# Kernel tuning notes

Hardware: AMD Instinct MI355X
Metric: run time of the kernel (lower is better)

Reference implementation:

```python
import jax, jax.numpy as jnp
import numpy as np

N = 50000
E = 800000
DIM = 64
MAX_DEG = 64
NUM_LAB = 16
BN_EPS = 1e-5
SLOPE = 0.01


def lrelu(x):
    return jnp.where(x > 0, x, SLOPE * x)


def batchnorm(x, w, b):
    m = x.mean(axis=0)
    v = x.var(axis=0)  # biased, matches torch BN normalization
    return (x - m) * jax.lax.rsqrt(v + BN_EPS) * w + b


def gin_conv(x, src, dst, wa, ba, wb, bb):
    # GINConv (eps=0): mlp(x + sum_{j->i} x_j); mlp = lin -> lrelu -> lin
    agg = jax.ops.segment_sum(x[src], dst, num_segments=x.shape[0])
    h = x + agg
    h = lrelu(h @ wa.T + ba)
    return h @ wb.T + bb


def setup_inputs() -> dict:
    key = jax.random.key(0)
    ks = iter(jax.random.split(key, 64))
    f = lambda *s: (jax.random.normal(next(ks), s, dtype=jnp.float32) * 0.1)
    dims = [2 * DIM, DIM, DIM, DIM]  # [128,64,64,64]
    inp = {
        'emb_deg': f(MAX_DEG, DIM),
        'emb_lab': f(NUM_LAB, DIM),
    }
    for i, (n1, n2) in enumerate(zip(dims[:-1], dims[1:])):
        inp[f'w{i}a'] = f(n1, n1)
        inp[f'b{i}a'] = f(n1)
        inp[f'w{i}b'] = f(n2, n1)
        inp[f'b{i}b'] = f(n2)
        inp[f'bn{i}_w'] = f(n2) + 1.0
        inp[f'bn{i}_b'] = f(n2)
    S = sum(dims)  # 320
    inp['fc1_w'] = f(DIM, S)
    inp['fc1_b'] = f(DIM)
    inp['fcbn_w'] = f(DIM) + 1.0
    inp['fcbn_b'] = f(DIM)
    inp['fc2_w'] = f(1, DIM)
    inp['fc2_b'] = f(1)
    inp['node_deg'] = jax.random.randint(next(ks), (N,), 0, MAX_DEG)
    inp['node_lab'] = jax.random.randint(next(ks), (N,), 0, NUM_LAB)
    inp['edge_index'] = jax.random.randint(next(ks), (2, E), 0, N)
    return inp


def reference(emb_deg, emb_lab,
              w0a, b0a, w0b, b0b, bn0_w, bn0_b,
              w1a, b1a, w1b, b1b, bn1_w, bn1_b,
              w2a, b2a, w2b, b2b, bn2_w, bn2_b,
              fc1_w, fc1_b, fcbn_w, fcbn_b, fc2_w, fc2_b,
              node_deg, node_lab, edge_index):
    src, dst = edge_index[0], edge_index[1]
    x0 = jnp.concatenate([emb_deg[node_deg], emb_lab[node_lab]], axis=1)  # [N, 2*DIM]
    z = [x0]
    layers = [(w0a, b0a, w0b, b0b, bn0_w, bn0_b),
              (w1a, b1a, w1b, b1b, bn1_w, bn1_b),
              (w2a, b2a, w2b, b2b, bn2_w, bn2_b)]
    for wa, ba, wb, bb, gw, gb in layers:
        x = gin_conv(z[-1], src, dst, wa, ba, wb, bb)
        x = lrelu(batchnorm(x, gw, gb))
        z.append(x)
    x = jnp.concatenate(z, axis=1)  # [N, sum(dims)]
    h = x @ fc1_w.T + fc1_b
    h = lrelu(batchnorm(h, fcbn_w, fcbn_b))
    out = jax.nn.sigmoid(h @ fc2_w.T + fc2_b)
    return out.squeeze(-1)  # [N]
```

## Files before the change

kernel.cpp:

```cpp
#include <hip/hip_runtime.h>

#define N_NODES 50000
#define E_EDGES 800000
#define BN_EPS 1e-5f
#define SLOPE 0.01f

#define SCAN_CHUNK 2048
#define SCAN_BLOCKS ((N_NODES + SCAN_CHUNK - 1) / SCAN_CHUNK)
#define STAT_SHARDS 32

typedef unsigned short ushort_t;
typedef unsigned int uint_t;
typedef short short8 __attribute__((ext_vector_type(8)));
typedef float floatx4 __attribute__((ext_vector_type(4)));

__device__ __forceinline__ float ulo(uint_t v) { return __uint_as_float(v << 16); }
__device__ __forceinline__ float uhi(uint_t v) { return __uint_as_float(v & 0xffff0000u); }
__device__ __forceinline__ ushort_t f2b(float f) {
    uint_t u = __float_as_uint(f);
    return (ushort_t)((u + 0x7fffu + ((u >> 16) & 1u)) >> 16);
}
__device__ __forceinline__ uint_t pack2(float a, float b) {
    return (uint_t)f2b(a) | ((uint_t)f2b(b) << 16);
}

#define OWA0 0
#define OWB0 16384
#define OWA1 24576
#define OWB1 28672
#define OWA2 32768
#define OWB2 36864
#define OFC1 40960
#define WTOT 61440
#define CVT_BLOCKS ((WTOT + 255) / 256)
#define P_BLOCKS 48

__global__ void k_prep(const float* __restrict__ wa0, const float* __restrict__ wb0,
                       const float* __restrict__ wa1, const float* __restrict__ wb1,
                       const float* __restrict__ wa2, const float* __restrict__ wb2,
                       const float* __restrict__ fc1w, ushort_t* __restrict__ dst,
                       const float* __restrict__ ed, const float* __restrict__ el,
                       ushort_t* __restrict__ Pt) {
    int b = blockIdx.x, t = threadIdx.x;
    if (b < CVT_BLOCKS) {
        int i = b * 256 + t;
        if (i >= WTOT) return;
        float v;
        if      (i < OWB0) v = wa0[i];
        else if (i < OWA1) v = wb0[i - OWB0];
        else if (i < OWB1) v = wa1[i - OWA1];
        else if (i < OWA2) v = wb1[i - OWB1];
        else if (i < OWB2) v = wa2[i - OWA2];
        else if (i < OFC1) v = wb2[i - OWB2];
        else               v = fc1w[i - OFC1];
        dst[i] = f2b(v);
    } else {
        int pid = (b - CVT_BLOCKS) * 256 + t;
        int c = pid >> 7, j = pid & 127;
        float acc = 0.f;
        if (c < 64) {
            const float* dr = ed + c * 64;
            const float* wr = wa0 + (size_t)j * 128;
            #pragma unroll 8
            for (int k = 0; k < 64; ++k) acc += dr[k] * wr[k];
        } else if (c < 80) {
            const float* dr = el + (c - 64) * 64;
            const float* wr = wa0 + (size_t)j * 128 + 64;
            #pragma unroll 8
            for (int k = 0; k < 64; ++k) acc += dr[k] * wr[k];
        }
        Pt[(size_t)j * 96 + c] = f2b(acc);
    }
}

__global__ void k_build_x0(const float* __restrict__ ed, const float* __restrict__ el,
                           const int* __restrict__ nd, const int* __restrict__ nl,
                           uint_t* __restrict__ x0u, int* __restrict__ ncls) {
    int idx = blockIdx.x * blockDim.x + threadIdx.x;
    if (idx >= N_NODES * 64) return;
    int n = idx >> 6, c = idx & 63;
    int d = nd[n], l = nl[n];
    if (c == 0) ncls[n] = d | (l << 16);
    float2 v = (c < 32) ? *(const float2*)(ed + d * 64 + c * 2)
                        : *(const float2*)(el + l * 64 + (c - 32) * 2);
    x0u[(size_t)n * 64 + c] = pack2(v.x, v.y);
}

__global__ void k_deg(const int* __restrict__ dst, int* __restrict__ deg) {
    int e = blockIdx.x * blockDim.x + threadIdx.x;
    if (e >= E_EDGES) return;
    atomicAdd(&deg[dst[e]], 1);
}

__global__ __launch_bounds__(256) void k_scan_a(const int* __restrict__ deg,
                                                int* __restrict__ bsum) {
    __shared__ int wsum[4];
    int t = threadIdx.x, b = blockIdx.x;
    int base = b * SCAN_CHUNK + t * 8;
    int s = 0;
    #pragma unroll
    for (int i = 0; i < 8; ++i) {
        int idx = base + i;
        if (idx < N_NODES) s += deg[idx];
    }
    #pragma unroll
    for (int o = 32; o; o >>= 1) s += __shfl_down(s, o);
    if ((t & 63) == 0) wsum[t >> 6] = s;
    __syncthreads();
    if (t == 0) bsum[b] = wsum[0] + wsum[1] + wsum[2] + wsum[3];
}

__global__ void k_scan_b(const int* __restrict__ bsum, int* __restrict__ bofs) {
    int t = threadIdx.x;
    int v = (t < SCAN_BLOCKS) ? bsum[t] : 0;
    int inc = v;
    #pragma unroll
    for (int o = 1; o < 32; o <<= 1) {
        int u = __shfl_up(inc, o, 32);
        if ((t & 31) >= o) inc += u;
    }
    if (t < SCAN_BLOCKS) bofs[t] = inc - v;
}

__global__ __launch_bounds__(256) void k_scan_c(const int* __restrict__ deg,
        const int* __restrict__ bofs, int* __restrict__ rowptr, int* __restrict__ wptr) {
    __shared__ int part[256];
    int t = threadIdx.x, b = blockIdx.x;
    int base = b * SCAN_CHUNK + t * 8;
    int vals[8];
    int s = 0;
    #pragma unroll
    for (int i = 0; i < 8; ++i) {
        int idx = base + i;
        vals[i] = (idx < N_NODES) ? deg[idx] : 0;
        s += vals[i];
    }
    part[t] = s;
    __syncthreads();
    #pragma unroll
    for (int off = 1; off < 256; off <<= 1) {
        int v = (t >= off) ? part[t - off] : 0;
        __syncthreads();
        part[t] += v;
        __syncthreads();
    }
    int run = bofs[b] + part[t] - s;
    #pragma unroll
    for (int i = 0; i < 8; ++i) {
        int idx = base + i;
        if (idx < N_NODES) {
            rowptr[idx] = run;
            wptr[idx]   = run;
            run += vals[i];
        }
    }
}

__global__ void k_fill(const int* __restrict__ src, const int* __restrict__ dst,
                       const int* __restrict__ ncls,
                       int* __restrict__ wptr, int* __restrict__ epk) {
    int e = blockIdx.x * blockDim.x + threadIdx.x;
    if (e >= E_EDGES) return;
    int s = src[e];
    int c = ncls[s];
    int pos = atomicAdd(&wptr[dst[e]], 1);
    epk[pos] = s | ((c & 63) << 16) | ((c >> 16) << 22);
}

__global__ __launch_bounds__(256, 8) void k_mlp0(
        const int* __restrict__ rowptr, const int* __restrict__ cdeg,
        const int* __restrict__ epk, const int* __restrict__ ncls,
        const ushort_t* __restrict__ Pt, const float* __restrict__ ba,
        const ushort_t* __restrict__ wbB, const float* __restrict__ bb,
        float* __restrict__ ybuf, float* __restrict__ stat_l) {
    constexpr int LHS = 98;
    constexpr int LDC = 104;
    constexpr int LDH = 136;
    __shared__ int hist[16 * LHS];
    __shared__ ushort_t xs[16 * LDC];
    __shared__ ushort_t hs[16 * LDH];
    uint_t* xsu = (uint_t*)xs;
    int t = threadIdx.x;
    int row0 = blockIdx.x * 16;
    int lane = t & 63, wv = t >> 6;
    int half = lane >> 5, hl = lane & 31;

    for (int i = t; i < 16 * LHS; i += 256) hist[i] = 0;
    __syncthreads();

    for (int i = 0; i < 2; ++i) {
        int lr = wv * 4 + i * 2 + half, node = row0 + lr;
        if (node < N_NODES) {
            if (hl == 0) {
                int c = ncls[node];
                atomicAdd(&hist[lr * LHS + (c & 0xffff)], 1);
                atomicAdd(&hist[lr * LHS + 64 + (c >> 16)], 1);
            }
            int start = rowptr[node], n = cdeg[node];
            for (int j0 = 0; j0 < n; j0 += 32) {
                int m = n - j0; if (m > 32) m = 32;
                if (hl < m) {
                    int ev = epk[start + j0 + hl];
                    atomicAdd(&hist[lr * LHS + ((ev >> 16) & 63)], 1);
                    atomicAdd(&hist[lr * LHS + 64 + ((ev >> 22) & 15)], 1);
                }
            }
        }
    }
    __syncthreads();

    for (int i = t; i < 16 * 48; i += 256) {
        int row = i / 48, c2 = i % 48;
        uint_t v = 0;
        if (c2 < 40)
            v = pack2((float)hist[row * LHS + c2 * 2],
                      (float)hist[row * LHS + c2 * 2 + 1]);
        xsu[row * 52 + c2] = v;
    }
    __syncthreads();

    int m = lane & 15, quad = lane >> 4;

    {
        floatx4 acc[2];
        acc[0] = (floatx4){0.f, 0.f, 0.f, 0.f};
        acc[1] = (floatx4){0.f, 0.f, 0.f, 0.f};
        #pragma unroll
        for (int ks = 0; ks < 3; ++ks) {
            short8 af = *(const short8*)(xs + m * LDC + ks * 32 + quad * 8);
            #pragma unroll
            for (int g = 0; g < 2; ++g) {
                int col = (wv * 2 + g) * 16 + m;
                short8 bf = *(const short8*)(Pt + (size_t)col * 96 + ks * 32 + quad * 8);
                acc[g] = __builtin_amdgcn_mfma_f32_16x16x32_bf16(af, bf, acc[g], 0, 0, 0);
            }
        }
        #pragma unroll
        for (int g = 0; g < 2; ++g) {
            int col = (wv * 2 + g) * 16 + m;
            float bias = ba[col];
            #pragma unroll
            for (int r = 0; r < 4; ++r) {
                float v = acc[g][r] + bias;
                v = v > 0.f ? v : SLOPE * v;
                hs[(quad * 4 + r) * LDH + col] = f2b(v);
            }
        }
    }
    __syncthreads();

    {
        floatx4 acc = (floatx4){0.f, 0.f, 0.f, 0.f};
        int col = wv * 16 + m;
        #pragma unroll
        for (int ks = 0; ks < 4; ++ks) {
            short8 af = *(const short8*)(hs + m * LDH + ks * 32 + quad * 8);
            short8 bf = *(const short8*)(wbB + (size_t)col * 128 + ks * 32 + quad * 8);
            acc = __builtin_amdgcn_mfma_f32_16x16x32_bf16(af, bf, acc, 0, 0, 0);
        }
        float bias = bb[col];
        float ps = 0.f, pq = 0.f;
        #pragma unroll
        for (int r = 0; r < 4; ++r) {
            int node = row0 + quad * 4 + r;
            float v = acc[r] + bias;
            if (node < N_NODES) ybuf[(size_t)node * 64 + col] = v;
            else v = 0.f;
            ps += v; pq += v * v;
        }
        ps += __shfl_xor(ps, 16); pq += __shfl_xor(pq, 16);
        ps += __shfl_xor(ps, 32); pq += __shfl_xor(pq, 32);
        if (quad == 0) {
            float* st = stat_l + (blockIdx.x & (STAT_SHARDS - 1)) * 128;
            atomicAdd(&st[col], ps);
            atomicAdd(&st[64 + col], pq);
        }
    }
}

__global__ __launch_bounds__(256, 8) void k_mlp64(
        const ushort_t* __restrict__ xb,
        const int* __restrict__ rowptr, const int* __restrict__ cdeg,
        const int* __restrict__ epk,
        const ushort_t* __restrict__ waB, const float* __restrict__ ba,
        const ushort_t* __restrict__ wbB, const float* __restrict__ bb,
        float* __restrict__ ybuf, float* __restrict__ stat_l) {
    constexpr int LDWB = 72;
    __shared__ ushort_t xs[16 * LDWB];
    __shared__ ushort_t hs[16 * LDWB];
    int t = threadIdx.x;
    int row0 = blockIdx.x * 16;
    int lane = t & 63, wv = t >> 6;
    int half = lane >> 5, hl = lane & 31;
    uint_t* xsu = (uint_t*)xs;
    const uint_t* xu = (const uint_t*)xb;

    for (int i = 0; i < 2; ++i) {
        int lr = wv * 4 + i * 2 + half, node = row0 + lr;
        float a0 = 0.f, a1 = 0.f, b0 = 0.f, b1 = 0.f;
        float c0 = 0.f, c1 = 0.f, d0 = 0.f, d1 = 0.f;
        float e0 = 0.f, e1 = 0.f, f0 = 0.f, f1 = 0.f;
        float g0 = 0.f, g1 = 0.f, h0 = 0.f, h1 = 0.f;
        if (node < N_NODES) {
            int start = rowptr[node], n = cdeg[node];
            uint_t sv = xu[(size_t)node * 32 + hl];
            a0 = ulo(sv); a1 = uhi(sv);
            for (int j0 = 0; j0 < n; j0 += 32) {
                int m = n - j0; if (m > 32) m = 32;
                int ev = (hl < m) ? epk[start + j0 + hl] : 0;
                int j = 0;
                for (; j + 8 <= m; j += 8) {
                    int s0 = __shfl(ev, j, 32) & 0xffff, s1 = __shfl(ev, j + 1, 32) & 0xffff;
                    int s2 = __shfl(ev, j + 2, 32) & 0xffff, s3 = __shfl(ev, j + 3, 32) & 0xffff;
                    int s4 = __shfl(ev, j + 4, 32) & 0xffff, s5 = __shfl(ev, j + 5, 32) & 0xffff;
                    int s6 = __shfl(ev, j + 6, 32) & 0xffff, s7 = __shfl(ev, j + 7, 32) & 0xffff;
                    uint_t v0 = xu[(size_t)s0 * 32 + hl];
                    uint_t v1 = xu[(size_t)s1 * 32 + hl];
                    uint_t v2 = xu[(size_t)s2 * 32 + hl];
                    uint_t v3 = xu[(size_t)s3 * 32 + hl];
                    uint_t v4 = xu[(size_t)s4 * 32 + hl];
                    uint_t v5 = xu[(size_t)s5 * 32 + hl];
                    uint_t v6 = xu[(size_t)s6 * 32 + hl];
                    uint_t v7 = xu[(size_t)s7 * 32 + hl];
                    a0 += ulo(v0); a1 += uhi(v0); b0 += ulo(v1); b1 += uhi(v1);
                    c0 += ulo(v2); c1 += uhi(v2); d0 += ulo(v3); d1 += uhi(v3);
                    e0 += ulo(v4); e1 += uhi(v4); f0 += ulo(v5); f1 += uhi(v5);
                    g0 += ulo(v6); g1 += uhi(v6); h0 += ulo(v7); h1 += uhi(v7);
                }
                for (; j < m; ++j) {
                    int s0 = __shfl(ev, j, 32) & 0xffff;
                    uint_t v0 = xu[(size_t)s0 * 32 + hl];
                    a0 += ulo(v0); a1 += uhi(v0);
                }
            }
        }
        float lo = ((a0 + b0) + (c0 + d0)) + ((e0 + f0) + (g0 + h0));
        float hi = ((a1 + b1) + (c1 + d1)) + ((e1 + f1) + (g1 + h1));
        xsu[lr * (LDWB / 2) + hl] = pack2(lo, hi);
    }
    __syncthreads();

    int m = lane & 15, quad = lane >> 4;

    {
        floatx4 acc = (floatx4){0.f, 0.f, 0.f, 0.f};
        int col = wv * 16 + m;
        #pragma unroll
        for (int ks = 0; ks < 2; ++ks) {
            short8 af = *(const short8*)(xs + m * LDWB + ks * 32 + quad * 8);
            short8 bf = *(const short8*)(waB + (size_t)col * 64 + ks * 32 + quad * 8);
            acc = __builtin_amdgcn_mfma_f32_16x16x32_bf16(af, bf, acc, 0, 0, 0);
        }
        float bias = ba[col];
        #pragma unroll
        for (int r = 0; r < 4; ++r) {
            float v = acc[r] + bias;
            v = v > 0.f ? v : SLOPE * v;
            hs[(quad * 4 + r) * LDWB + col] = f2b(v);
        }
    }
    __syncthreads();

    {
        floatx4 acc = (floatx4){0.f, 0.f, 0.f, 0.f};
        int col = wv * 16 + m;
        #pragma unroll
        for (int ks = 0; ks < 2; ++ks) {
            short8 af = *(const short8*)(hs + m * LDWB + ks * 32 + quad * 8);
            short8 bf = *(const short8*)(wbB + (size_t)col * 64 + ks * 32 + quad * 8);
            acc = __builtin_amdgcn_mfma_f32_16x16x32_bf16(af, bf, acc, 0, 0, 0);
        }
        float bias = bb[col];
        float ps = 0.f, pq = 0.f;
        #pragma unroll
        for (int r = 0; r < 4; ++r) {
            int node = row0 + quad * 4 + r;
            float v = acc[r] + bias;
            if (node < N_NODES) ybuf[(size_t)node * 64 + col] = v;
            else v = 0.f;
            ps += v; pq += v * v;
        }
        ps += __shfl_xor(ps, 16); pq += __shfl_xor(pq, 16);
        ps += __shfl_xor(ps, 32); pq += __shfl_xor(pq, 32);
        if (quad == 0) {
            float* st = stat_l + (blockIdx.x & (STAT_SHARDS - 1)) * 128;
            atomicAdd(&st[col], ps);
            atomicAdd(&st[64 + col], pq);
        }
    }
}

__global__ void k_bn_apply(const float* __restrict__ y, const float* __restrict__ stat_l,
                           const float* __restrict__ gw, const float* __restrict__ gb,
                           uint_t* __restrict__ xo) {
    __shared__ float sc[64], sh[64];
    int t = threadIdx.x;
    if (t < 64) {
        float s0 = 0.f, q0 = 0.f;
        #pragma unroll
        for (int j = 0; j < STAT_SHARDS; ++j) {
            s0 += stat_l[j * 128 + t];
            q0 += stat_l[j * 128 + 64 + t];
        }
        float mmm = s0 * (1.0f / N_NODES);
        float var = q0 * (1.0f / N_NODES) - mmm * mmm;
        float s = gw[t] * rsqrtf(var + BN_EPS);
        sc[t] = s; sh[t] = gb[t] - mmm * s;
    }
    __syncthreads();
    int idx = blockIdx.x * blockDim.x + t;
    if (idx >= N_NODES * 16) return;
    int c4 = (idx & 15) * 4;
    float4 v4 = *(const float4*)(y + (size_t)idx * 4);
    float o0 = v4.x * sc[c4]     + sh[c4];     o0 = o0 > 0.f ? o0 : SLOPE * o0;
    float o1 = v4.y * sc[c4 + 1] + sh[c4 + 1]; o1 = o1 > 0.f ? o1 : SLOPE * o1;
    float o2 = v4.z * sc[c4 + 2] + sh[c4 + 2]; o2 = o2 > 0.f ? o2 : SLOPE * o2;
    float o3 = v4.w * sc[c4 + 3] + sh[c4 + 3]; o3 = o3 > 0.f ? o3 : SLOPE * o3;
    xo[(size_t)idx * 2]     = pack2(o0, o1);
    xo[(size_t)idx * 2 + 1] = pack2(o2, o3);
}

__global__ __launch_bounds__(256, 8) void k_fc1(
        const uint_t* __restrict__ x0u, const uint_t* __restrict__ x1u,
        const uint_t* __restrict__ x2u, const uint_t* __restrict__ x3u,
        const ushort_t* __restrict__ wB, const float* __restrict__ b,
        float* __restrict__ ybuf, float* __restrict__ stat_l) {
    constexpr int LDWB = 328;
    __shared__ ushort_t xs[16 * LDWB];
    uint_t* xsu = (uint_t*)xs;
    int t = threadIdx.x;
    int row0 = blockIdx.x * 16;

    for (int i = t; i < 16 * 160; i += 256) {
        int row = i / 160, c = i % 160;
        int g = row0 + row;
        uint_t v = 0;
        if (g < N_NODES) {
            if      (c < 64)  v = x0u[(size_t)g * 64 + c];
            else if (c < 96)  v = x1u[(size_t)g * 32 + (c - 64)];
            else if (c < 128) v = x2u[(size_t)g * 32 + (c - 96)];
            else              v = x3u[(size_t)g * 32 + (c - 128)];
        }
        xsu[row * 164 + c] = v;
    }
    __syncthreads();

    int lane = t & 63, wv = t >> 6;
    int m = lane & 15, quad = lane >> 4;
    int col = wv * 16 + m;
    floatx4 acc = (floatx4){0.f, 0.f, 0.f, 0.f};
    #pragma unroll
    for (int ks = 0; ks < 10; ++ks) {
        short8 af = *(const short8*)(xs + m * LDWB + ks * 32 + quad * 8);
        short8 bf = *(const short8*)(wB + (size_t)col * 320 + ks * 32 + quad * 8);
        acc = __builtin_amdgcn_mfma_f32_16x16x32_bf16(af, bf, acc, 0, 0, 0);
    }
    float bias = b[col];
    float ps = 0.f, pq = 0.f;
    #pragma unroll
    for (int r = 0; r < 4; ++r) {
        int node = row0 + quad * 4 + r;
        float v = acc[r] + bias;
        if (node < N_NODES) ybuf[(size_t)node * 64 + col] = v;
        else v = 0.f;
        ps += v; pq += v * v;
    }
    ps += __shfl_xor(ps, 16); pq += __shfl_xor(pq, 16);
    ps += __shfl_xor(ps, 32); pq += __shfl_xor(pq, 32);
    if (quad == 0) {
        float* st = stat_l + (blockIdx.x & (STAT_SHARDS - 1)) * 128;
        atomicAdd(&st[col], ps);
        atomicAdd(&st[64 + col], pq);
    }
}

__global__ void k_final(const float* __restrict__ y, const float* __restrict__ stat_l,
                        const float* __restrict__ gw, const float* __restrict__ gb,
                        const float* __restrict__ w2, const float* __restrict__ b2,
                        float* __restrict__ out) {
    __shared__ float sc[64], sh[64], w[64];
    int t = threadIdx.x;
    if (t < 64) {
        float s0 = 0.f, q0 = 0.f;
        #pragma unroll
        for (int j = 0; j < STAT_SHARDS; ++j) {
            s0 += stat_l[j * 128 + t];
            q0 += stat_l[j * 128 + 64 + t];
        }
        float mmm = s0 * (1.0f / N_NODES);
        float var = q0 * (1.0f / N_NODES) - mmm * mmm;
        float s = gw[t] * rsqrtf(var + BN_EPS);
        sc[t] = s; sh[t] = gb[t] - mmm * s; w[t] = w2[t];
    }
    __syncthreads();
    int i = blockIdx.x * blockDim.x + t;
    if (i >= N_NODES) return;
    float z = b2[0];
    const float* row = y + (size_t)i * 64;
    #pragma unroll
    for (int c = 0; c < 64; c += 4) {
        float4 v4 = *(const float4*)(row + c);
        float v;
        v = v4.x * sc[c]   + sh[c];   v = v > 0.f ? v : SLOPE * v; z += v * w[c];
        v = v4.y * sc[c+1] + sh[c+1]; v = v > 0.f ? v : SLOPE * v; z += v * w[c+1];
        v = v4.z * sc[c+2] + sh[c+2]; v = v > 0.f ? v : SLOPE * v; z += v * w[c+2];
        v = v4.w * sc[c+3] + sh[c+3]; v = v > 0.f ? v : SLOPE * v; z += v * w[c+3];
    }
    out[i] = 1.f / (1.f + __expf(-z));
}

extern "C" void kernel_launch(void* const* d_in, const int* in_sizes, int n_in,
                              void* d_out, int out_size, void* d_ws, size_t ws_size,
                              hipStream_t stream) {
    const float* emb_deg = (const float*)d_in[0];
    const float* emb_lab = (const float*)d_in[1];
    const float* wA[3]  = {(const float*)d_in[2],  (const float*)d_in[8],  (const float*)d_in[14]};
    const float* bA[3]  = {(const float*)d_in[3],  (const float*)d_in[9],  (const float*)d_in[15]};
    const float* wB[3]  = {(const float*)d_in[4],  (const float*)d_in[10], (const float*)d_in[16]};
    const float* bB[3]  = {(const float*)d_in[5],  (const float*)d_in[11], (const float*)d_in[17]};
    const float* bnw[3] = {(const float*)d_in[6],  (const float*)d_in[12], (const float*)d_in[18]};
    const float* bnb[3] = {(const float*)d_in[7],  (const float*)d_in[13], (const float*)d_in[19]};
    const float* fc1_w  = (const float*)d_in[20];
    const float* fc1_b  = (const float*)d_in[21];
    const float* fcbn_w = (const float*)d_in[22];
    const float* fcbn_b = (const float*)d_in[23];
    const float* fc2_w  = (const float*)d_in[24];
    const float* fc2_b  = (const float*)d_in[25];
    const int* node_deg = (const int*)d_in[26];
    const int* node_lab = (const int*)d_in[27];
    const int* src = (const int*)d_in[28];
    const int* dst = src + E_EDGES;
    float* out = (float*)d_out;

    float* ws   = (float*)d_ws;
    float* ybf  = ws;
    float* stat = ybf + (size_t)N_NODES * 64;
    uint_t* x0u = (uint_t*)(stat + 4 * STAT_SHARDS * 128);
    uint_t* x1u = x0u + (size_t)N_NODES * 64;
    uint_t* x2u = x1u + (size_t)N_NODES * 32;
    uint_t* x3u = x2u + (size_t)N_NODES * 32;
    int* epk    = (int*)(x3u + (size_t)N_NODES * 32);
    ushort_t* wbf = (ushort_t*)(epk + E_EDGES);
    ushort_t* Ptb = wbf + WTOT;
    int* cdeg   = (int*)(Ptb + 128 * 96);
    int* rowptr = cdeg + N_NODES;
    int* wptr   = rowptr + N_NODES;
    int* ncls   = wptr + N_NODES;
    int* bsum   = ncls + N_NODES;
    int* bofs   = bsum + SCAN_BLOCKS;

    const int RB = (N_NODES + 15) / 16;
    const int VB = (N_NODES * 16 + 255) / 256;
    const int HB = (N_NODES * 64 + 255) / 256;
    const int EB = (E_EDGES + 255) / 256;
    const int NB = (N_NODES + 255) / 256;

    hipMemsetAsync(stat, 0, (size_t)(4 * STAT_SHARDS * 128) * sizeof(float), stream);
    hipMemsetAsync(cdeg, 0, (size_t)N_NODES * sizeof(int), stream);

    k_prep<<<CVT_BLOCKS + P_BLOCKS, 256, 0, stream>>>(wA[0], wB[0], wA[1], wB[1],
        wA[2], wB[2], fc1_w, wbf, emb_deg, emb_lab, Ptb);
    k_build_x0<<<HB, 256, 0, stream>>>(emb_deg, emb_lab, node_deg, node_lab, x0u, ncls);

    k_deg<<<EB, 256, 0, stream>>>(dst, cdeg);
    k_scan_a<<<SCAN_BLOCKS, 256, 0, stream>>>(cdeg, bsum);
    k_scan_b<<<1, 64, 0, stream>>>(bsum, bofs);
    k_scan_c<<<SCAN_BLOCKS, 256, 0, stream>>>(cdeg, bofs, rowptr, wptr);
    k_fill<<<EB, 256, 0, stream>>>(src, dst, ncls, wptr, epk);

    k_mlp0<<<RB, 256, 0, stream>>>(rowptr, cdeg, epk, ncls, Ptb, bA[0],
                                   wbf + OWB0, bB[0], ybf, stat);
    k_bn_apply<<<VB, 256, 0, stream>>>(ybf, stat, bnw[0], bnb[0], x1u);

    uint_t* xin[4] = {x0u, x1u, x2u, x3u};
    const ushort_t* waOfs[3] = {wbf + OWA0, wbf + OWA1, wbf + OWA2};
    const ushort_t* wbOfs[3] = {wbf + OWB0, wbf + OWB1, wbf + OWB2};
    for (int l = 1; l < 3; ++l) {
        float* st = stat + l * STAT_SHARDS * 128;
        k_mlp64<<<RB, 256, 0, stream>>>((const ushort_t*)xin[l], rowptr, cdeg, epk,
            waOfs[l], bA[l], wbOfs[l], bB[l], ybf, st);
        k_bn_apply<<<VB, 256, 0, stream>>>(ybf, st, bnw[l], bnb[l], xin[l + 1]);
    }

    float* stf = stat + 3 * STAT_SHARDS * 128;
    k_fc1<<<RB, 256, 0, stream>>>(x0u, x1u, x2u, x3u, wbf + OFC1, fc1_b, ybf, stf);
    k_final<<<NB, 256, 0, stream>>>(ybf, stf, fcbn_w, fcbn_b, fc2_w, fc2_b, out);
}
```

Baseline: 351.1 us.

## Rank edges during degree count, fold scan_b, vectorize neighbor gather

The degree-count kernel now records each edge's rank within its destination, so the fill kernel writes CSR slots without a second atomic. Fill is split into destination-range passes to localize scattered writes. The separate block-offset scan kernel is folded into scan_c. The 64-wide layer gather now loads 16-byte vectors per lane with four edges in flight and reduces across lane groups with shuffles. The cost is an extra rank array and eight passes that each re-read dst.

```diff
diff --git a/kernel.cpp b/kernel.cpp
--- a/kernel.cpp
+++ b/kernel.cpp
@@ -8,6 +8,7 @@
 #define SCAN_CHUNK 2048
 #define SCAN_BLOCKS ((N_NODES + SCAN_CHUNK - 1) / SCAN_CHUNK)
 #define STAT_SHARDS 32
+#define FILL_PASSES 8
 
 typedef unsigned short ushort_t;
 typedef unsigned int uint_t;
@@ -86,10 +87,11 @@
     x0u[(size_t)n * 64 + c] = pack2(v.x, v.y);
 }
 
-__global__ void k_deg(const int* __restrict__ dst, int* __restrict__ deg) {
+__global__ void k_degrank(const int* __restrict__ dst, int* __restrict__ deg,
+                          int* __restrict__ rank) {
     int e = blockIdx.x * blockDim.x + threadIdx.x;
     if (e >= E_EDGES) return;
-    atomicAdd(&deg[dst[e]], 1);
+    rank[e] = atomicAdd(&deg[dst[e]], 1);
 }
 
 __global__ __launch_bounds__(256) void k_scan_a(const int* __restrict__ deg,
@@ -110,22 +112,17 @@
     if (t == 0) bsum[b] = wsum[0] + wsum[1] + wsum[2] + wsum[3];
 }
 
-__global__ void k_scan_b(const int* __restrict__ bsum, int* __restrict__ bofs) {
-    int t = threadIdx.x;
-    int v = (t < SCAN_BLOCKS) ? bsum[t] : 0;
-    int inc = v;
-    #pragma unroll
-    for (int o = 1; o < 32; o <<= 1) {
-        int u = __shfl_up(inc, o, 32);
-        if ((t & 31) >= o) inc += u;
-    }
-    if (t < SCAN_BLOCKS) bofs[t] = inc - v;
-}
-
 __global__ __launch_bounds__(256) void k_scan_c(const int* __restrict__ deg,
-        const int* __restrict__ bofs, int* __restrict__ rowptr, int* __restrict__ wptr) {
+        const int* __restrict__ bsum, int* __restrict__ rowptr) {
     __shared__ int part[256];
+    __shared__ int blockofs;
     int t = threadIdx.x, b = blockIdx.x;
+    if (t < 64) {
+        int v = (t < b) ? bsum[t] : 0;
+        #pragma unroll
+        for (int o = 32; o; o >>= 1) v += __shfl_down(v, o);
+        if (t == 0) blockofs = v;
+    }
     int base = b * SCAN_CHUNK + t * 8;
     int vals[8];
     int s = 0;
@@ -144,27 +141,31 @@
         part[t] += v;
         __syncthreads();
     }
-    int run = bofs[b] + part[t] - s;
+    int run = blockofs + part[t] - s;
     #pragma unroll
     for (int i = 0; i < 8; ++i) {
         int idx = base + i;
         if (idx < N_NODES) {
             rowptr[idx] = run;
-            wptr[idx]   = run;
             run += vals[i];
         }
     }
 }
 
 __global__ void k_fill(const int* __restrict__ src, const int* __restrict__ dst,
-                       const int* __restrict__ ncls,
-                       int* __restrict__ wptr, int* __restrict__ epk) {
-    int e = blockIdx.x * blockDim.x + threadIdx.x;
+                       const int* __restrict__ ncls, const int* __restrict__ rowptr,
+                       const int* __restrict__ rank, int* __restrict__ epk,
+                       int blocks_per_pass) {
+    int p = blockIdx.x / blocks_per_pass;
+    int e = (blockIdx.x % blocks_per_pass) * blockDim.x + threadIdx.x;
     if (e >= E_EDGES) return;
+    int d = dst[e];
+    const int span = (N_NODES + FILL_PASSES - 1) / FILL_PASSES;
+    int lo = p * span;
+    if (d < lo || d >= lo + span) return;
     int s = src[e];
     int c = ncls[s];
-    int pos = atomicAdd(&wptr[dst[e]], 1);
-    epk[pos] = s | ((c & 63) << 16) | ((c >> 16) << 22);
+    epk[rowptr[d] + rank[e]] = s | ((c & 63) << 16) | ((c >> 16) << 22);
 }
 
 __global__ __launch_bounds__(256, 8) void k_mlp0(
@@ -292,51 +293,61 @@
     int row0 = blockIdx.x * 16;
     int lane = t & 63, wv = t >> 6;
     int half = lane >> 5, hl = lane & 31;
-    uint_t* xsu = (uint_t*)xs;
-    const uint_t* xu = (const uint_t*)xb;
+    int g = hl >> 3, sseg = hl & 7;
+    const uint4* xu4 = (const uint4*)xb;
 
     for (int i = 0; i < 2; ++i) {
         int lr = wv * 4 + i * 2 + half, node = row0 + lr;
-        float a0 = 0.f, a1 = 0.f, b0 = 0.f, b1 = 0.f;
-        float c0 = 0.f, c1 = 0.f, d0 = 0.f, d1 = 0.f;
-        float e0 = 0.f, e1 = 0.f, f0 = 0.f, f1 = 0.f;
-        float g0 = 0.f, g1 = 0.f, h0 = 0.f, h1 = 0.f;
+        float acc[8] = {0.f, 0.f, 0.f, 0.f, 0.f, 0.f, 0.f, 0.f};
         if (node < N_NODES) {
             int start = rowptr[node], n = cdeg[node];
-            uint_t sv = xu[(size_t)node * 32 + hl];
-            a0 = ulo(sv); a1 = uhi(sv);
+            if (g == 0) {
+                uint4 v = xu4[(size_t)node * 8 + sseg];
+                acc[0] += ulo(v.x); acc[1] += uhi(v.x);
+                acc[2] += ulo(v.y); acc[3] += uhi(v.y);
+                acc[4] += ulo(v.z); acc[5] += uhi(v.z);
+                acc[6] += ulo(v.w); acc[7] += uhi(v.w);
+            }
             for (int j0 = 0; j0 < n; j0 += 32) {
                 int m = n - j0; if (m > 32) m = 32;
                 int ev = (hl < m) ? epk[start + j0 + hl] : 0;
                 int j = 0;
                 for (; j + 8 <= m; j += 8) {
-                    int s0 = __shfl(ev, j, 32) & 0xffff, s1 = __shfl(ev, j + 1, 32) & 0xffff;
-                    int s2 = __shfl(ev, j + 2, 32) & 0xffff, s3 = __shfl(ev, j + 3, 32) & 0xffff;
-                    int s4 = __shfl(ev, j + 4, 32) & 0xffff, s5 = __shfl(ev, j + 5, 32) & 0xffff;
-                    int s6 = __shfl(ev, j + 6, 32) & 0xffff, s7 = __shfl(ev, j + 7, 32) & 0xffff;
-                    uint_t v0 = xu[(size_t)s0 * 32 + hl];
-                    uint_t v1 = xu[(size_t)s1 * 32 + hl];
-                    uint_t v2 = xu[(size_t)s2 * 32 + hl];
-                    uint_t v3 = xu[(size_t)s3 * 32 + hl];
-                    uint_t v4 = xu[(size_t)s4 * 32 + hl];
-                    uint_t v5 = xu[(size_t)s5 * 32 + hl];
-                    uint_t v6 = xu[(size_t)s6 * 32 + hl];
-                    uint_t v7 = xu[(size_t)s7 * 32 + hl];
-                    a0 += ulo(v0); a1 += uhi(v0); b0 += ulo(v1); b1 += uhi(v1);
-                    c0 += ulo(v2); c1 += uhi(v2); d0 += ulo(v3); d1 += uhi(v3);
-                    e0 += ulo(v4); e1 += uhi(v4); f0 += ulo(v5); f1 += uhi(v5);
-                    g0 += ulo(v6); g1 += uhi(v6); h0 += ulo(v7); h1 += uhi(v7);
+                    int sa = __shfl(ev, j + g, 32) & 0xffff;
+                    int sb = __shfl(ev, j + 4 + g, 32) & 0xffff;
+                    uint4 va = xu4[(size_t)sa * 8 + sseg];
+                    uint4 vb = xu4[(size_t)sb * 8 + sseg];
+                    acc[0] += ulo(va.x); acc[1] += uhi(va.x);
+                    acc[2] += ulo(va.y); acc[3] += uhi(va.y);
+                    acc[4] += ulo(va.z); acc[5] += uhi(va.z);
+                    acc[6] += ulo(va.w); acc[7] += uhi(va.w);
+                    acc[0] += ulo(vb.x); acc[1] += uhi(vb.x);
+                    acc[2] += ulo(vb.y); acc[3] += uhi(vb.y);
+                    acc[4] += ulo(vb.z); acc[5] += uhi(vb.z);
+                    acc[6] += ulo(vb.w); acc[7] += uhi(vb.w);
                 }
-                for (; j < m; ++j) {
-                    int s0 = __shfl(ev, j, 32) & 0xffff;
-                    uint_t v0 = xu[(size_t)s0 * 32 + hl];
-                    a0 += ulo(v0); a1 += uhi(v0);
+                for (; j < m; j += 4) {
+                    int sa = __shfl(ev, j + g, 32) & 0xffff;
+                    if (g < m - j) {
+                        uint4 va = xu4[(size_t)sa * 8 + sseg];
+                        acc[0] += ulo(va.x); acc[1] += uhi(va.x);
+                        acc[2] += ulo(va.y); acc[3] += uhi(va.y);
+                        acc[4] += ulo(va.z); acc[5] += uhi(va.z);
+                        acc[6] += ulo(va.w); acc[7] += uhi(va.w);
+                    }
                 }
             }
         }
-        float lo = ((a0 + b0) + (c0 + d0)) + ((e0 + f0) + (g0 + h0));
-        float hi = ((a1 + b1) + (c1 + d1)) + ((e1 + f1) + (g1 + h1));
-        xsu[lr * (LDWB / 2) + hl] = pack2(lo, hi);
+        #pragma unroll
+        for (int q = 0; q < 8; ++q) {
+            acc[q] += __shfl_xor(acc[q], 8, 32);
+            acc[q] += __shfl_xor(acc[q], 16, 32);
+        }
+        if (g == 0) {
+            uint4 pv = make_uint4(pack2(acc[0], acc[1]), pack2(acc[2], acc[3]),
+                                  pack2(acc[4], acc[5]), pack2(acc[6], acc[7]));
+            *(uint4*)(xs + lr * LDWB + sseg * 8) = pv;
+        }
     }
     __syncthreads();
 
@@ -540,14 +551,13 @@
     uint_t* x2u = x1u + (size_t)N_NODES * 32;
     uint_t* x3u = x2u + (size_t)N_NODES * 32;
     int* epk    = (int*)(x3u + (size_t)N_NODES * 32);
-    ushort_t* wbf = (ushort_t*)(epk + E_EDGES);
+    int* rank   = epk + E_EDGES;
+    ushort_t* wbf = (ushort_t*)(rank + E_EDGES);
     ushort_t* Ptb = wbf + WTOT;
     int* cdeg   = (int*)(Ptb + 128 * 96);
     int* rowptr = cdeg + N_NODES;
-    int* wptr   = rowptr + N_NODES;
-    int* ncls   = wptr + N_NODES;
+    int* ncls   = rowptr + N_NODES;
     int* bsum   = ncls + N_NODES;
-    int* bofs   = bsum + SCAN_BLOCKS;
 
     const int RB = (N_NODES + 15) / 16;
     const int VB = (N_NODES * 16 + 255) / 256;
@@ -562,11 +572,10 @@
         wA[2], wB[2], fc1_w, wbf, emb_deg, emb_lab, Ptb);
     k_build_x0<<<HB, 256, 0, stream>>>(emb_deg, emb_lab, node_deg, node_lab, x0u, ncls);
 
-    k_deg<<<EB, 256, 0, stream>>>(dst, cdeg);
+    k_degrank<<<EB, 256, 0, stream>>>(dst, cdeg, rank);
     k_scan_a<<<SCAN_BLOCKS, 256, 0, stream>>>(cdeg, bsum);
-    k_scan_b<<<1, 64, 0, stream>>>(bsum, bofs);
-    k_scan_c<<<SCAN_BLOCKS, 256, 0, stream>>>(cdeg, bofs, rowptr, wptr);
-    k_fill<<<EB, 256, 0, stream>>>(src, dst, ncls, wptr, epk);
+    k_scan_c<<<SCAN_BLOCKS, 256, 0, stream>>>(cdeg, bsum, rowptr);
+    k_fill<<<FILL_PASSES * EB, 256, 0, stream>>>(src, dst, ncls, rowptr, rank, epk, EB);
 
     k_mlp0<<<RB, 256, 0, stream>>>(rowptr, cdeg, epk, ncls, Ptb, bA[0],
                                    wbf + OWB0, bB[0], ybf, stat);
```

Measured after the change: 319.5 us. 1.1x faster.
